# Performance work log

Measured on AMD Instinct MI355X. Metric: run time of the kernel, lower is better.

The kernel has to match this reference:

```python
import jax, jax.numpy as jnp
import numpy as np

N_NODES = 100_000
E_OFF = 1_000_000
HID = 32
GF = 8
NF = 8
N_LAYERS = 3


def _mlp(h, W1, b1, W2, b2):
    # Linear -> ReLU -> Linear (matches MLP([in, hidden, out]))
    return jax.nn.relu(h @ W1 + b1) @ W2 + b2


def _seg_mean(v, idx, n):
    s = jax.ops.segment_sum(v, idx, num_segments=n)
    c = jax.ops.segment_sum(jnp.ones((v.shape[0], 1), v.dtype), idx, num_segments=n)
    return s / jnp.maximum(c, 1.0)


def _graphnet(x, row, col, eattr2, g, p):
    # GraphNet with global block: edge MLP -> mean-aggregate to nodes -> node MLP -> global MLP
    eW1, eb1, eW2, eb2, nW1, nb1, nW2, nb2, gW1, gb1, gW2, gb2 = p
    n, e = x.shape[0], row.shape[0]
    gE = jnp.broadcast_to(g, (e, g.shape[1]))
    e_emb = _mlp(jnp.concatenate([gE, x[row], x[col], eattr2], axis=1), eW1, eb1, eW2, eb2)
    agg = _seg_mean(e_emb, row, n)
    gN = jnp.broadcast_to(g, (n, g.shape[1]))
    n_emb = _mlp(jnp.concatenate([gN, x, agg], axis=1), nW1, nb1, nW2, nb2)
    g_new = _mlp(jnp.concatenate([n_emb.mean(0, keepdims=True), e_emb.mean(0, keepdims=True), g], axis=1),
                 gW1, gb1, gW2, gb2)
    return e_emb, n_emb, g_new


def setup_inputs() -> dict:
    key = jax.random.key(0)
    ks = jax.random.split(key, 24)
    a = jax.random.randint(ks[0], (E_OFF,), 0, N_NODES)
    b = jax.random.randint(ks[1], (E_OFF,), 0, N_NODES)
    d = jnp.arange(N_NODES)
    l_ei = jnp.stack([jnp.concatenate([jnp.maximum(a, b), d]),
                      jnp.concatenate([jnp.minimum(a, b), d])])  # lower triangular + diag
    c = jax.random.randint(ks[2], (E_OFF,), 0, N_NODES)
    e = jax.random.randint(ks[3], (E_OFF,), 0, N_NODES)
    u_ei = jnp.stack([jnp.concatenate([jnp.minimum(c, e), d]),
                      jnp.concatenate([jnp.maximum(c, e), d])])  # upper triangular + diag
    E = E_OFF + N_NODES
    x = jax.random.normal(ks[4], (N_NODES, NF), dtype=jnp.float32)
    l_attr = jax.random.normal(ks[5], (E, 1), dtype=jnp.float32)
    u_attr = jax.random.normal(ks[6], (E, 1), dtype=jnp.float32)

    def w(k, shape):
        return (jax.random.normal(k, shape, dtype=jnp.float32) / np.sqrt(shape[-2])).astype(jnp.float32)

    e_in = GF + 2 * NF + 1 + 1  # 26 (edge attr padded to 2: skip col, zeros where absent)
    n_in = GF + 1 + NF          # 17
    g_in = NF + 1 + GF          # 17
    return {
        'x': x, 'l_edge_index': l_ei, 'u_edge_index': u_ei,
        'l_edge_attr': l_attr, 'u_edge_attr': u_attr,
        'eW1': w(ks[7], (2, N_LAYERS, e_in, HID)), 'eb1': 0.01 * jax.random.normal(ks[8], (2, N_LAYERS, HID)),
        'eW2': w(ks[9], (2, N_LAYERS, HID, 1)), 'eb2': 0.01 * jax.random.normal(ks[10], (2, N_LAYERS, 1)),
        'nW1': w(ks[11], (2, N_LAYERS, n_in, HID)), 'nb1': 0.01 * jax.random.normal(ks[12], (2, N_LAYERS, HID)),
        'nW2': w(ks[13], (2, N_LAYERS, HID, NF)), 'nb2': 0.01 * jax.random.normal(ks[14], (2, N_LAYERS, NF)),
        'gW1': w(ks[15], (2, N_LAYERS, g_in, HID)), 'gb1': 0.01 * jax.random.normal(ks[16], (2, N_LAYERS, HID)),
        'gW2': w(ks[17], (2, N_LAYERS, HID, GF)), 'gb2': 0.01 * jax.random.normal(ks[18], (2, N_LAYERS, GF)),
    }


def reference(x, l_edge_index, u_edge_index, l_edge_attr, u_edge_attr,
              eW1, eb1, eW2, eb2, nW1, nb1, nW2, nb2, gW1, gb1, gW2, gb2):
    params = (eW1, eb1, eW2, eb2, nW1, nb1, nW2, nb2, gW1, gb1, gW2, gb2)
    lr, lc = l_edge_index[0], l_edge_index[1]
    ur, uc = u_edge_index[0], u_edge_index[1]
    g = jnp.zeros((1, GF), x.dtype)
    l_e, u_e = l_edge_attr, u_edge_attr
    l_a = l_edge_attr  # skip-connection edge features (original matrix values)
    zl, zu = jnp.zeros_like(l_edge_attr), jnp.zeros_like(u_edge_attr)
    for i in range(N_LAYERS):
        p1 = tuple(w[0, i] for w in params)
        p2 = tuple(w[1, i] for w in params)
        l_in = jnp.concatenate([l_e, l_a if i != 0 else zl], axis=1)  # zeros col == no skip (block 0)
        l_e, l_n, g = _graphnet(x, lr, lc, l_in, g, p1)
        u_in = jnp.concatenate([u_e, zu], axis=1)  # l2 never has skip; padded zeros col
        u_e, u_n, g = _graphnet(l_n, ur, uc, u_in, g, p2)
        # NOTE: node embeddings are NOT carried across MP blocks in the original
    l_vals = jnp.where(lr == lc, jnp.exp(l_e[:, 0]), l_e[:, 0])
    u_vals = jnp.where(ur == uc, jnp.exp(u_e[:, 0]), u_e[:, 0])
    return jnp.concatenate([l_vals, u_vals])
```

## Files before the change

kernel.cpp:

```cpp
#include <hip/hip_runtime.h>


typedef unsigned int u32;

#define NB_SHIFT 9
#define NB_SIZE 512
#define RSTRIDE 1104

__device__ __forceinline__ float wave_sum(float v) {
#pragma unroll
    for (int off = 32; off > 0; off >>= 1) v += __shfl_down(v, off, 64);
    return v;
}


__global__ __launch_bounds__(256) void hist_kernel(
    const int* __restrict__ lr, const int* __restrict__ ur,
    u32* __restrict__ hist, int E, int B) {
    __shared__ u32 h[256];
    const int t = threadIdx.x;
    if (t < B) h[t] = 0;
    __syncthreads();
    const int s = blockIdx.y;
    const int* rows = s ? ur : lr;
    for (int i = blockIdx.x * 256 + t; i < E; i += gridDim.x * 256)
        atomicAdd(&h[rows[i] >> NB_SHIFT], 1u);
    __syncthreads();
    if (t < B && h[t]) atomicAdd(&hist[s * B + t], h[t]);
}

__global__ __launch_bounds__(256) void scan_kernel(
    const u32* __restrict__ hist, u32* __restrict__ offs,
    u32* __restrict__ cur, int B) {
    __shared__ u32 sh[256];
    const int t = threadIdx.x;
    for (int s = 0; s < 2; ++s) {
        const u32 v = (t < B) ? hist[s * B + t] : 0u;
        sh[t] = v;
        __syncthreads();
#pragma unroll
        for (int off = 1; off < 256; off <<= 1) {
            const u32 add = (t >= off) ? sh[t - off] : 0u;
            __syncthreads();
            sh[t] += add;
            __syncthreads();
        }
        const u32 exc = sh[t] - v;
        if (t < B) {
            offs[s * (B + 1) + t] = exc;
            cur[s * B + t] = exc;
        }
        if (t == 255) offs[s * (B + 1) + B] = sh[255];
        __syncthreads();
    }
}

#define SCHUNK 4096
__global__ __launch_bounds__(256) void scatter_kernel(
    const int* __restrict__ lr, const int* __restrict__ ur,
    const int* __restrict__ lc, const int* __restrict__ uc,
    const float* __restrict__ la, const float* __restrict__ ua,
    u32* __restrict__ cur, int4* __restrict__ pk, u32* __restrict__ inv,
    int E, int B) {
    __shared__ u32 lcnt[256], lbase[256];
    const int t = threadIdx.x;
    const int s = blockIdx.y;
    const int* rows = s ? ur : lr;
    const int* cols = s ? uc : lc;
    const float* attr = s ? ua : la;
    int4* mypk = pk + (size_t)s * E;
    u32* myinv = inv + (size_t)s * E;
    if (t < B) lcnt[t] = 0;
    __syncthreads();
    const int base_e = blockIdx.x * SCHUNK;
#pragma unroll
    for (int k = 0; k < SCHUNK / 256; ++k) {
        const int e = base_e + k * 256 + t;
        if (e < E) atomicAdd(&lcnt[rows[e] >> NB_SHIFT], 1u);
    }
    __syncthreads();
    if (t < B) {
        const u32 c = lcnt[t];
        lbase[t] = c ? atomicAdd(&cur[s * B + t], c) : 0u;
        lcnt[t] = 0;
    }
    __syncthreads();
#pragma unroll
    for (int k = 0; k < SCHUNK / 256; ++k) {
        const int e = base_e + k * 256 + t;
        if (e < E) {
            const int rv = rows[e];
            const int b = rv >> NB_SHIFT;
            const u32 pos = lbase[b] + atomicAdd(&lcnt[b], 1u);
            mypk[pos] = make_int4(rv, cols[e], __float_as_int(attr[e]), 0);
            myinv[e] = pos;
        }
    }
}


template <bool SKIP, bool GAGG, bool VALS, bool STORE, bool GCOMP, bool EPF2>
__global__ __launch_bounds__(256, 3) void edge_kernel(
    const float4* __restrict__ xf,
    const int4* __restrict__ pk,
    const float2* __restrict__ eprevf2,
    const float* __restrict__ W1,
    const float* __restrict__ b1,
    const float* __restrict__ W2,
    const float* __restrict__ b2,
    const float* __restrict__ gprev,
    float* __restrict__ gout,
    const float* __restrict__ pebins,
    const float* __restrict__ pnbins,
    const float* __restrict__ gW1, const float* __restrict__ gb1,
    const float* __restrict__ gW2, const float* __restrict__ gb2,
    float* __restrict__ ebins,
    float2* __restrict__ e_out,
    float* __restrict__ vsort,
    int E, int N, float inv_E) {
    __shared__ float gsh[8];
    __shared__ float biasE[32];
    __shared__ float wpart[4];
    const int t = threadIdx.x;
    if constexpr (GCOMP) {
        if (t < 64) {
            float nb[8];
#pragma unroll
            for (int q = 0; q < 8; ++q) nb[q] = pnbins[t * 16 + q];
            const float eb = pebins[t];
            float gin[17];
#pragma unroll
            for (int q = 0; q < 8; ++q) {
                const float s = wave_sum(nb[q]);
                gin[q] = __shfl(s, 0, 64) / (float)N;
            }
            const float es = wave_sum(eb);
            gin[8] = __shfl(es, 0, 64) * inv_E;
#pragma unroll
            for (int k = 0; k < 8; ++k) gin[9 + k] = gprev[k];
            float hv = 0.0f;
            if (t < 32) {
                hv = gb1[t];
#pragma unroll
                for (int k = 0; k < 17; ++k)
                    hv = fmaf(gin[k], gW1[k * 32 + t], hv);
                hv = fmaxf(hv, 0.0f);
            }
#pragma unroll
            for (int q = 0; q < 8; ++q) {
                const float c = (t < 32) ? hv * gW2[t * 8 + q] : 0.0f;
                const float s = wave_sum(c);
                if (t == 0) {
                    const float gv = gb2[q] + s;
                    gsh[q] = gv;
                    if (blockIdx.x == 0) gout[q] = gv;
                }
            }
        }
    } else {
        if (t < 8) gsh[t] = gprev[t];
    }
    __syncthreads();
    if (t < 32) {
        float v = b1[t];
#pragma unroll
        for (int k = 0; k < 8; ++k) v = fmaf(gsh[k], W1[k * 32 + t], v);
        biasE[t] = v;
    }
    __syncthreads();

    const int e = blockIdx.x * 256 + t;
    const bool valid = e < E;
    const int idx = valid ? e : 0;
    const int4 p = pk[idx];
    const int r = p.x;
    const int c = p.y;
    const float attr = __int_as_float(p.z);
    float epv;
    if constexpr (EPF2) epv = eprevf2[idx].x;
    else epv = attr;
    const float4 xr0 = xf[2 * r], xr1 = xf[2 * r + 1];
    const float4 xc0 = xf[2 * c], xc1 = xf[2 * c + 1];
    float in[18] = {xr0.x, xr0.y, xr0.z, xr0.w, xr1.x, xr1.y, xr1.z, xr1.w,
                    xc0.x, xc0.y, xc0.z, xc0.w, xc1.x, xc1.y, xc1.z, xc1.w,
                    epv, 0.0f};
    if constexpr (SKIP) in[17] = attr;

    float h[32];
#pragma unroll
    for (int q = 0; q < 8; ++q) {
        const float4 b = reinterpret_cast<const float4*>(biasE)[q];
        h[4 * q + 0] = b.x; h[4 * q + 1] = b.y;
        h[4 * q + 2] = b.z; h[4 * q + 3] = b.w;
    }
    const float4* __restrict__ W4 =
        reinterpret_cast<const float4*>(W1 + 8 * 32);
#pragma unroll
    for (int k = 0; k < 18; ++k) {
        const float v = in[k];
#pragma unroll
        for (int q = 0; q < 8; ++q) {
            const float4 w = W4[k * 8 + q];
            h[4 * q + 0] = fmaf(v, w.x, h[4 * q + 0]);
            h[4 * q + 1] = fmaf(v, w.y, h[4 * q + 1]);
            h[4 * q + 2] = fmaf(v, w.z, h[4 * q + 2]);
            h[4 * q + 3] = fmaf(v, w.w, h[4 * q + 3]);
        }
    }
    float out = b2[0];
    const float4* __restrict__ W24 = reinterpret_cast<const float4*>(W2);
#pragma unroll
    for (int q = 0; q < 8; ++q) {
        const float4 w = W24[q];
        out = fmaf(fmaxf(h[4 * q + 0], 0.f), w.x, out);
        out = fmaf(fmaxf(h[4 * q + 1], 0.f), w.y, out);
        out = fmaf(fmaxf(h[4 * q + 2], 0.f), w.z, out);
        out = fmaf(fmaxf(h[4 * q + 3], 0.f), w.w, out);
    }

    if (valid) {
        if constexpr (STORE)
            e_out[e] = make_float2(out, __int_as_float(r & (NB_SIZE - 1)));
        if constexpr (VALS) vsort[e] = (r == c) ? expf(out) : out;
    }
    if constexpr (GAGG) {
        const float s = wave_sum(valid ? out : 0.0f);
        if ((t & 63) == 0) wpart[t >> 6] = s;
        __syncthreads();
        if (t == 0)
            atomicAdd(&ebins[blockIdx.x & 63],
                      wpart[0] + wpart[1] + wpart[2] + wpart[3]);
    }
}


template <bool COUNT, bool STORE_N>
__global__ __launch_bounds__(1024) void aggnode_kernel(
    const u32* __restrict__ offs,
    const float2* __restrict__ em,
    const float4* __restrict__ xf,
    float* __restrict__ cntf,
    const float* __restrict__ g,
    const float* __restrict__ nW1, const float* __restrict__ nb1,
    const float* __restrict__ nW2, const float* __restrict__ nb2,
    float* __restrict__ n_out,
    float* __restrict__ nbins,
    int N) {
    __shared__ float sbin[NB_SIZE];
    __shared__ float cbin[NB_SIZE];
    __shared__ float biasN[32];
    __shared__ float npart[8][8];
    const int t = threadIdx.x;
    if (t < NB_SIZE) {
        sbin[t] = 0.0f;
        if constexpr (COUNT) cbin[t] = 0.0f;
    }
    if (t >= NB_SIZE && t < NB_SIZE + 32) {
        const int j = t - NB_SIZE;
        float v = nb1[j];
#pragma unroll
        for (int k = 0; k < 8; ++k) v = fmaf(g[k], nW1[k * 32 + j], v);
        biasN[j] = v;
    }
    __syncthreads();
    const int b = blockIdx.x;
    const u32 beg = offs[b], end = offs[b + 1];
    for (u32 i = beg + t; i < end; i += 1024) {
        const float2 v = em[i];
        const int rl = __float_as_int(v.y);
        atomicAdd(&sbin[rl], v.x);
        if constexpr (COUNT) atomicAdd(&cbin[rl], 1.0f);
    }
    __syncthreads();

    const int n0 = b << NB_SHIFT;
    float o[8];
    const bool active = (t < NB_SIZE) && (n0 + t < N);
    if (t < NB_SIZE) {
        const int n = n0 + t;
        const int idx = active ? n : (N - 1);
        float cntv;
        if constexpr (COUNT) {
            cntv = cbin[t];
            if (active) cntf[n] = cntv;
        } else {
            cntv = cntf[idx];
        }
        const float agg = sbin[t] / fmaxf(cntv, 1.0f);
        const float4 x0 = xf[2 * idx], x1 = xf[2 * idx + 1];
        float in[9] = {x0.x, x0.y, x0.z, x0.w, x1.x, x1.y, x1.z, x1.w, agg};
        float h[32];
#pragma unroll
        for (int j = 0; j < 8; ++j) {
            const float4 bb = reinterpret_cast<const float4*>(biasN)[j];
            h[4 * j + 0] = bb.x; h[4 * j + 1] = bb.y;
            h[4 * j + 2] = bb.z; h[4 * j + 3] = bb.w;
        }
        const float* __restrict__ Wk = nW1 + 8 * 32;
#pragma unroll
        for (int k = 0; k < 9; ++k) {
            const float v = in[k];
#pragma unroll
            for (int j = 0; j < 32; ++j) h[j] = fmaf(v, Wk[k * 32 + j], h[j]);
        }
#pragma unroll
        for (int q = 0; q < 8; ++q) o[q] = nb2[q];
#pragma unroll
        for (int j = 0; j < 32; ++j) {
            const float hv = fmaxf(h[j], 0.0f);
#pragma unroll
            for (int q = 0; q < 8; ++q) o[q] = fmaf(hv, nW2[j * 8 + q], o[q]);
        }
        if constexpr (STORE_N) {
            if (active) {
                reinterpret_cast<float4*>(n_out)[2 * n] =
                    make_float4(o[0], o[1], o[2], o[3]);
                reinterpret_cast<float4*>(n_out)[2 * n + 1] =
                    make_float4(o[4], o[5], o[6], o[7]);
            }
        }
#pragma unroll
        for (int q = 0; q < 8; ++q) {
            const float s = wave_sum(active ? o[q] : 0.0f);
            if ((t & 63) == 0) npart[t >> 6][q] = s;
        }
    }
    __syncthreads();
    if (t < 8) {
        float a = 0.0f;
#pragma unroll
        for (int w = 0; w < 8; ++w) a += npart[w][t];
        atomicAdd(&nbins[(b & 63) * 16 + t], a);
    }
}


__global__ __launch_bounds__(256) void unperm_kernel(
    const float* __restrict__ vs,
    const u32* __restrict__ inv,
    float* __restrict__ out, int E) {
    const int i = blockIdx.x * 256 + threadIdx.x;
    if (i < 2 * E) {
        const u32 p = inv[i];
        out[i] = (i < E) ? vs[p] : vs[E + p];
    }
}

extern "C" void kernel_launch(void* const* d_in, const int* in_sizes, int n_in,
                              void* d_out, int out_size, void* d_ws,
                              size_t ws_size, hipStream_t stream) {
    const float* x = (const float*)d_in[0];
    const int* l_ei = (const int*)d_in[1];
    const int* u_ei = (const int*)d_in[2];
    const float* l_attr = (const float*)d_in[3];
    const float* u_attr = (const float*)d_in[4];
    const float* eW1 = (const float*)d_in[5];
    const float* eb1 = (const float*)d_in[6];
    const float* eW2 = (const float*)d_in[7];
    const float* eb2 = (const float*)d_in[8];
    const float* nW1 = (const float*)d_in[9];
    const float* nb1 = (const float*)d_in[10];
    const float* nW2 = (const float*)d_in[11];
    const float* nb2 = (const float*)d_in[12];
    const float* gW1 = (const float*)d_in[13];
    const float* gb1 = (const float*)d_in[14];
    const float* gW2 = (const float*)d_in[15];
    const float* gb2 = (const float*)d_in[16];

    const int E = in_sizes[3];
    const int N = in_sizes[0] / 8;
    const int B = (N + NB_SIZE - 1) >> NB_SHIFT;

    float* ws = (float*)d_ws;
    int4* pk = (int4*)ws;
    float* l_e = ws + (size_t)8 * E;
    float* u_e = l_e + (size_t)2 * E;
    float* vs = u_e + (size_t)2 * E;
    u32* inv = (u32*)(vs + (size_t)2 * E);
    float* l_n = (float*)(inv + (size_t)2 * E);
    float* cnt_l = l_n + (size_t)8 * N;
    float* cnt_u = cnt_l + N;
    float* gslot = cnt_u + N;
    u32* hist = (u32*)(gslot + 56);
    float* dyn_all = (float*)(hist + 2 * B);
    u32* offs = (u32*)(dyn_all + 5 * RSTRIDE);
    u32* cur = offs + 2 * (B + 1);

    const int* lr = l_ei;
    const int* lc = l_ei + E;
    const int* ur = u_ei;
    const int* uc = u_ei + E;
    const int eg = (E + 255) / 256;
    const int sg = (E + SCHUNK - 1) / SCHUNK;
    const float invE = 1.0f / (float)E;
    float* outAll = (float*)d_out;
    const u32* offs_l = offs;
    const u32* offs_u = offs + (B + 1);

    hipMemsetAsync(gslot, 0, (size_t)(56 + 2 * B + 5 * RSTRIDE) * sizeof(float),
                   stream);
    hist_kernel<<<dim3(128, 2), 256, 0, stream>>>(lr, ur, hist, E, B);
    scan_kernel<<<1, 256, 0, stream>>>(hist, offs, cur, B);
    scatter_kernel<<<dim3(sg, 2), 256, 0, stream>>>(lr, ur, lc, uc, l_attr,
                                                    u_attr, cur, pk, inv, E, B);

    const size_t wsl[6] = {0, 3, 1, 4, 2, 5};

    for (int j = 0; j < 6; ++j) {
        const bool lower = !(j & 1);
        const size_t sl = wsl[j];
        float* ebins = dyn_all + (size_t)(j <= 4 ? j : 4) * RSTRIDE;
        float* nbins = ebins + 64;
        const float* pe = (j >= 1) ? dyn_all + (size_t)(j - 1) * RSTRIDE : nullptr;
        const float* pn = (j >= 1) ? pe + 64 : nullptr;
        const size_t psl = (j >= 1) ? wsl[j - 1] : 0;
        const float4* exf = (const float4*)(lower ? x : l_n);
        const int4* pks = lower ? pk : pk + E;
        const float2* eprevf2 =
            (const float2*)(lower ? l_e : u_e);
        float2* e_out = (float2*)(lower ? l_e : u_e);
        float* vsort = lower ? vs : vs + E;
        const float* gprev = gslot + (size_t)(j >= 1 ? j - 1 : 0) * 8;
        float* gout = gslot + (size_t)j * 8;

#define EDGE_ARGS                                                             \
    exf, pks, eprevf2, eW1 + sl * 832, eb1 + sl * 32, eW2 + sl * 32,          \
        eb2 + sl, gprev, gout, pe, pn, gW1 + psl * 544, gb1 + psl * 32,       \
        gW2 + psl * 256, gb2 + psl * 8, ebins, e_out, vsort, E, N, invE

        switch (j) {
            case 0: edge_kernel<false, true, false, true, false, false>
                        <<<eg, 256, 0, stream>>>(EDGE_ARGS); break;
            case 1: edge_kernel<false, true, false, true, true, false>
                        <<<eg, 256, 0, stream>>>(EDGE_ARGS); break;
            case 2: edge_kernel<true, true, false, true, true, true>
                        <<<eg, 256, 0, stream>>>(EDGE_ARGS); break;
            case 3: edge_kernel<false, true, false, true, true, true>
                        <<<eg, 256, 0, stream>>>(EDGE_ARGS); break;
            case 4: edge_kernel<true, true, true, true, true, true>
                        <<<eg, 256, 0, stream>>>(EDGE_ARGS); break;
            case 5: edge_kernel<false, false, true, false, true, true>
                        <<<eg, 256, 0, stream>>>(EDGE_ARGS); break;
        }
#undef EDGE_ARGS

        if (j == 5) break;

        const u32* aoffs = lower ? offs_l : offs_u;
        float* cntf = lower ? cnt_l : cnt_u;
        const float4* nxf = (const float4*)(lower ? x : l_n);
        const float2* em = (const float2*)(lower ? l_e : u_e);

#define AGG_ARGS                                                              \
    aoffs, em, nxf, cntf, gslot + (size_t)j * 8, nW1 + sl * 544,              \
        nb1 + sl * 32, nW2 + sl * 256, nb2 + sl * 8, l_n, nbins, N

        switch (j) {
            case 0: aggnode_kernel<true, true>
                        <<<B, 1024, 0, stream>>>(AGG_ARGS); break;
            case 1: aggnode_kernel<true, false>
                        <<<B, 1024, 0, stream>>>(AGG_ARGS); break;
            case 2: aggnode_kernel<false, true>
                        <<<B, 1024, 0, stream>>>(AGG_ARGS); break;
            case 3: aggnode_kernel<false, false>
                        <<<B, 1024, 0, stream>>>(AGG_ARGS); break;
            case 4: aggnode_kernel<false, true>
                        <<<B, 1024, 0, stream>>>(AGG_ARGS); break;
        }
#undef AGG_ARGS
    }

    unperm_kernel<<<(2 * E + 255) / 256, 256, 0, stream>>>(vs, inv, outAll, E);
}
```

Before: 550.3 us.

## Precompute per-node first-layer projections and gather them in edge kernel

A new node-level kernel computes the row and column halves of the edge MLP's first layer for every node, x·W_row + bias and x·W_col. It also absorbs the global-MLP and bias computation previously done in each edge block. The edge kernel then only gathers two 32-float projections, adds the edge-attribute and skip terms, and applies ReLU and the output layer. This removes most of the per-edge FMAs. In exchange, each edge gathers 256 bytes instead of 64, a 64·N-float workspace buffer is added, and there is one extra launch per layer.

Measured after the change: 735.1 us. 33.6% more time.

```diff
diff --git a/kernel.cpp b/kernel.cpp
--- a/kernel.cpp
+++ b/kernel.cpp
@@ -99,28 +99,20 @@
 }
 
 
-template <bool SKIP, bool GAGG, bool VALS, bool STORE, bool GCOMP, bool EPF2>
-__global__ __launch_bounds__(256, 3) void edge_kernel(
+template <bool GCOMP>
+__global__ __launch_bounds__(256) void nodepre_kernel(
     const float4* __restrict__ xf,
-    const int4* __restrict__ pk,
-    const float2* __restrict__ eprevf2,
     const float* __restrict__ W1,
     const float* __restrict__ b1,
-    const float* __restrict__ W2,
-    const float* __restrict__ b2,
     const float* __restrict__ gprev,
     float* __restrict__ gout,
-    const float* __restrict__ pebins,
-    const float* __restrict__ pnbins,
+    const float* __restrict__ pebins, const float* __restrict__ pnbins,
     const float* __restrict__ gW1, const float* __restrict__ gb1,
     const float* __restrict__ gW2, const float* __restrict__ gb2,
-    float* __restrict__ ebins,
-    float2* __restrict__ e_out,
-    float* __restrict__ vsort,
-    int E, int N, float inv_E) {
+    float4* __restrict__ y,
+    int N, float inv_E) {
     __shared__ float gsh[8];
     __shared__ float biasE[32];
-    __shared__ float wpart[4];
     const int t = threadIdx.x;
     if constexpr (GCOMP) {
         if (t < 64) {
@@ -169,6 +161,47 @@
     }
     __syncthreads();
 
+    const int n = blockIdx.x * 256 + t;
+    if (n >= N) return;
+    const float4 x0 = xf[2 * n], x1 = xf[2 * n + 1];
+    const float xk[8] = {x0.x, x0.y, x0.z, x0.w, x1.x, x1.y, x1.z, x1.w};
+    const float4* __restrict__ W4 = reinterpret_cast<const float4*>(W1);
+    float4* __restrict__ yo = y + (size_t)n * 16;
+#pragma unroll
+    for (int q = 0; q < 8; ++q) {
+        float4 ar = reinterpret_cast<const float4*>(biasE)[q];
+        float4 ac = make_float4(0.f, 0.f, 0.f, 0.f);
+#pragma unroll
+        for (int k = 0; k < 8; ++k) {
+            const float4 wr = W4[(8 + k) * 8 + q];
+            const float4 wc = W4[(16 + k) * 8 + q];
+            const float v = xk[k];
+            ar.x = fmaf(v, wr.x, ar.x); ar.y = fmaf(v, wr.y, ar.y);
+            ar.z = fmaf(v, wr.z, ar.z); ar.w = fmaf(v, wr.w, ar.w);
+            ac.x = fmaf(v, wc.x, ac.x); ac.y = fmaf(v, wc.y, ac.y);
+            ac.z = fmaf(v, wc.z, ac.z); ac.w = fmaf(v, wc.w, ac.w);
+        }
+        yo[q] = ar;
+        yo[8 + q] = ac;
+    }
+}
+
+
+template <bool SKIP, bool GAGG, bool VALS, bool STORE, bool EPF2>
+__global__ __launch_bounds__(256) void edge_kernel(
+    const float4* __restrict__ y,
+    const int4* __restrict__ pk,
+    const float2* __restrict__ eprevf2,
+    const float* __restrict__ we,
+    const float* __restrict__ wsk,
+    const float* __restrict__ W2,
+    const float* __restrict__ b2,
+    float* __restrict__ ebins,
+    float2* __restrict__ e_out,
+    float* __restrict__ vsort,
+    int E) {
+    __shared__ float wpart[4];
+    const int t = threadIdx.x;
     const int e = blockIdx.x * 256 + t;
     const bool valid = e < E;
     const int idx = valid ? e : 0;
@@ -176,48 +209,38 @@
     const int r = p.x;
     const int c = p.y;
     const float attr = __int_as_float(p.z);
-    float epv;
-    if constexpr (EPF2) epv = eprevf2[idx].x;
-    else epv = attr;
-    const float4 xr0 = xf[2 * r], xr1 = xf[2 * r + 1];
-    const float4 xc0 = xf[2 * c], xc1 = xf[2 * c + 1];
-    float in[18] = {xr0.x, xr0.y, xr0.z, xr0.w, xr1.x, xr1.y, xr1.z, xr1.w,
-                    xc0.x, xc0.y, xc0.z, xc0.w, xc1.x, xc1.y, xc1.z, xc1.w,
-                    epv, 0.0f};
-    if constexpr (SKIP) in[17] = attr;
-
-    float h[32];
+    float ep;
+    if constexpr (EPF2) ep = eprevf2[idx].x;
+    else ep = attr;
+    const float4* __restrict__ yr = y + (size_t)r * 16;
+    const float4* __restrict__ yc = y + (size_t)c * 16 + 8;
+    const float4* __restrict__ we4 = reinterpret_cast<const float4*>(we);
+    const float4* __restrict__ ws4 = reinterpret_cast<const float4*>(wsk);
+    const float4* __restrict__ w24 = reinterpret_cast<const float4*>(W2);
+    float out = b2[0];
 #pragma unroll
     for (int q = 0; q < 8; ++q) {
-        const float4 b = reinterpret_cast<const float4*>(biasE)[q];
-        h[4 * q + 0] = b.x; h[4 * q + 1] = b.y;
-        h[4 * q + 2] = b.z; h[4 * q + 3] = b.w;
-    }
-    const float4* __restrict__ W4 =
-        reinterpret_cast<const float4*>(W1 + 8 * 32);
-#pragma unroll
-    for (int k = 0; k < 18; ++k) {
-        const float v = in[k];
-#pragma unroll
-        for (int q = 0; q < 8; ++q) {
-            const float4 w = W4[k * 8 + q];
-            h[4 * q + 0] = fmaf(v, w.x, h[4 * q + 0]);
-            h[4 * q + 1] = fmaf(v, w.y, h[4 * q + 1]);
-            h[4 * q + 2] = fmaf(v, w.z, h[4 * q + 2]);
-            h[4 * q + 3] = fmaf(v, w.w, h[4 * q + 3]);
-        }
-    }
-    float out = b2[0];
-    const float4* __restrict__ W24 = reinterpret_cast<const float4*>(W2);
-#pragma unroll
-    for (int q = 0; q < 8; ++q) {
-        const float4 w = W24[q];
-        out = fmaf(fmaxf(h[4 * q + 0], 0.f), w.x, out);
-        out = fmaf(fmaxf(h[4 * q + 1], 0.f), w.y, out);
-        out = fmaf(fmaxf(h[4 * q + 2], 0.f), w.z, out);
-        out = fmaf(fmaxf(h[4 * q + 3], 0.f), w.w, out);
-    }
-
+        const float4 a = yr[q];
+        const float4 b = yc[q];
+        const float4 w = we4[q];
+        float4 h;
+        h.x = fmaf(ep, w.x, a.x + b.x);
+        h.y = fmaf(ep, w.y, a.y + b.y);
+        h.z = fmaf(ep, w.z, a.z + b.z);
+        h.w = fmaf(ep, w.w, a.w + b.w);
+        if constexpr (SKIP) {
+            const float4 s = ws4[q];
+            h.x = fmaf(attr, s.x, h.x);
+            h.y = fmaf(attr, s.y, h.y);
+            h.z = fmaf(attr, s.z, h.z);
+            h.w = fmaf(attr, s.w, h.w);
+        }
+        const float4 w2 = w24[q];
+        out = fmaf(fmaxf(h.x, 0.f), w2.x, out);
+        out = fmaf(fmaxf(h.y, 0.f), w2.y, out);
+        out = fmaf(fmaxf(h.z, 0.f), w2.z, out);
+        out = fmaf(fmaxf(h.w, 0.f), w2.w, out);
+    }
     if (valid) {
         if constexpr (STORE)
             e_out[e] = make_float2(out, __int_as_float(r & (NB_SIZE - 1)));
@@ -336,8 +359,7 @@
 
 
 __global__ __launch_bounds__(256) void unperm_kernel(
-    const float* __restrict__ vs,
-    const u32* __restrict__ inv,
+    const float* __restrict__ vs, const u32* __restrict__ inv,
     float* __restrict__ out, int E) {
     const int i = blockIdx.x * 256 + threadIdx.x;
     if (i < 2 * E) {
@@ -378,7 +400,8 @@
     float* vs = u_e + (size_t)2 * E;
     u32* inv = (u32*)(vs + (size_t)2 * E);
     float* l_n = (float*)(inv + (size_t)2 * E);
-    float* cnt_l = l_n + (size_t)8 * N;
+    float* y = l_n + (size_t)8 * N;
+    float* cnt_l = y + (size_t)64 * N;
     float* cnt_u = cnt_l + N;
     float* gslot = cnt_u + N;
     u32* hist = (u32*)(gslot + 56);
@@ -391,6 +414,7 @@
     const int* ur = u_ei;
     const int* uc = u_ei + E;
     const int eg = (E + 255) / 256;
+    const int ng = (N + 255) / 256;
     const int sg = (E + SCHUNK - 1) / SCHUNK;
     const float invE = 1.0f / (float)E;
     float* outAll = (float*)d_out;
@@ -414,32 +438,40 @@
         const float* pe = (j >= 1) ? dyn_all + (size_t)(j - 1) * RSTRIDE : nullptr;
         const float* pn = (j >= 1) ? pe + 64 : nullptr;
         const size_t psl = (j >= 1) ? wsl[j - 1] : 0;
-        const float4* exf = (const float4*)(lower ? x : l_n);
+        const float4* nxf = (const float4*)(lower ? x : l_n);
         const int4* pks = lower ? pk : pk + E;
-        const float2* eprevf2 =
-            (const float2*)(lower ? l_e : u_e);
+        const float2* eprevf2 = (const float2*)(lower ? l_e : u_e);
         float2* e_out = (float2*)(lower ? l_e : u_e);
         float* vsort = lower ? vs : vs + E;
         const float* gprev = gslot + (size_t)(j >= 1 ? j - 1 : 0) * 8;
         float* gout = gslot + (size_t)j * 8;
+        const float* W1s = eW1 + sl * 832;
+
+#define NP_ARGS                                                               \
+    nxf, W1s, eb1 + sl * 32, gprev, gout, pe, pn, gW1 + psl * 544,            \
+        gb1 + psl * 32, gW2 + psl * 256, gb2 + psl * 8, (float4*)y, N, invE
+        if (j == 0)
+            nodepre_kernel<false><<<ng, 256, 0, stream>>>(NP_ARGS);
+        else
+            nodepre_kernel<true><<<ng, 256, 0, stream>>>(NP_ARGS);
+#undef NP_ARGS
 
 #define EDGE_ARGS                                                             \
-    exf, pks, eprevf2, eW1 + sl * 832, eb1 + sl * 32, eW2 + sl * 32,          \
-        eb2 + sl, gprev, gout, pe, pn, gW1 + psl * 544, gb1 + psl * 32,       \
-        gW2 + psl * 256, gb2 + psl * 8, ebins, e_out, vsort, E, N, invE
+    (const float4*)y, pks, eprevf2, W1s + 24 * 32, W1s + 25 * 32,             \
+        eW2 + sl * 32, eb2 + sl, ebins, e_out, vsort, E
 
         switch (j) {
-            case 0: edge_kernel<false, true, false, true, false, false>
+            case 0: edge_kernel<false, true, false, true, false>
                         <<<eg, 256, 0, stream>>>(EDGE_ARGS); break;
-            case 1: edge_kernel<false, true, false, true, true, false>
+            case 1: edge_kernel<false, true, false, true, false>
                         <<<eg, 256, 0, stream>>>(EDGE_ARGS); break;
-            case 2: edge_kernel<true, true, false, true, true, true>
+            case 2: edge_kernel<true, true, false, true, true>
                         <<<eg, 256, 0, stream>>>(EDGE_ARGS); break;
-            case 3: edge_kernel<false, true, false, true, true, true>
+            case 3: edge_kernel<false, true, false, true, true>
                         <<<eg, 256, 0, stream>>>(EDGE_ARGS); break;
-            case 4: edge_kernel<true, true, true, true, true, true>
+            case 4: edge_kernel<true, true, true, true, true>
                         <<<eg, 256, 0, stream>>>(EDGE_ARGS); break;
-            case 5: edge_kernel<false, false, true, false, true, true>
+            case 5: edge_kernel<false, false, true, false, true>
                         <<<eg, 256, 0, stream>>>(EDGE_ARGS); break;
         }
 #undef EDGE_ARGS
@@ -448,7 +480,6 @@
 
         const u32* aoffs = lower ? offs_l : offs_u;
         float* cntf = lower ? cnt_l : cnt_u;
-        const float4* nxf = (const float4*)(lower ? x : l_n);
         const float2* em = (const float2*)(lower ? l_e : u_e);
 
 #define AGG_ARGS                                                              \
```
